# Optimization experiments

Measured on AMD Instinct MI355X. Metric: run time of the kernel, lower is better.

Reference implementation:

```python
import jax, jax.numpy as jnp
import numpy as np

B = 256      # number of graphs (args.batch_size)
NPG = 1000   # nodes per graph (args.num_node)
C = 64       # in_channels
DEG = 16     # avg degree
K = 500      # ceil(ratio * NPG), ratio = 0.5
EPS = 1e-8


def setup_inputs() -> dict:
    key = jax.random.key(0)
    k1, k2, k3, k4, k5 = jax.random.split(key, 5)
    N = B * NPG
    epg = NPG * DEG  # edges per graph
    x = jax.random.normal(k1, (N, C), jnp.float32)
    src = jax.random.randint(k2, (B, epg), 0, NPG)
    dst = jax.random.randint(k3, (B, epg), 0, NPG)
    off = (jnp.arange(B, dtype=jnp.int32) * NPG)[:, None]
    edge_index = jnp.stack([(src + off).reshape(-1), (dst + off).reshape(-1)]).astype(jnp.int32)
    edge_attr = jax.random.uniform(k4, (B * epg,), jnp.float32)
    batch = jnp.repeat(jnp.arange(B, dtype=jnp.int32), NPG)
    W = jax.random.normal(k5, (C, C), jnp.float32) * (1.0 / np.sqrt(C))
    b = jnp.zeros((C,), jnp.float32)
    return {"istraining": 1, "x": x, "edge_index": edge_index, "edge_attr": edge_attr,
            "batch": batch, "W": W, "b": b}


def _gcn_conv(x, edge_index, W, b):
    # PyG GCNConv: x' = D^{-1/2} (A + I) D^{-1/2} X W + b, unit edge weights.
    N = x.shape[0]
    sl = jnp.arange(N, dtype=edge_index.dtype)
    src = jnp.concatenate([edge_index[0], sl])  # message source j
    dst = jnp.concatenate([edge_index[1], sl])  # aggregation target i
    deg = jnp.zeros((N,), x.dtype).at[dst].add(1.0)
    dinv = jnp.where(deg > 0, jax.lax.rsqrt(jnp.maximum(deg, 1.0)), 0.0)
    norm = dinv[src] * dinv[dst]          # [E+N]
    h = x @ W                              # [N, C]
    msg = h[src] * norm[:, None]           # gather + scale (dominant traffic)
    out = jax.ops.segment_sum(msg, dst, num_segments=N) + b
    return out


def _node_score(x):
    # compute_node_score: cosine similarity of each node to its graph centroid
    # (community prototype), plus KL(softmax(score) || uniform) per graph.
    xb = x.reshape(B, NPG, C)
    cen = xb.mean(axis=1, keepdims=True)                       # [B,1,C]
    num = jnp.sum(xb * cen, axis=-1)                           # [B,NPG]
    den = jnp.linalg.norm(xb, axis=-1) * jnp.linalg.norm(cen, axis=-1) + EPS
    score = num / den                                          # [B,NPG]
    logp = jax.nn.log_softmax(score, axis=1)
    kl = jnp.sum(jnp.exp(logp) * (logp + jnp.log(jnp.float32(NPG))), axis=1)  # [B]
    indices_ = jnp.argsort(-score, axis=1)                     # [B,NPG]
    return score, kl, indices_


def reference(istraining, x, edge_index, edge_attr, batch, W, b):
    N = x.shape[0]
    x = _gcn_conv(x, edge_index, W, b)
    score, kl_all_batch, indices_ = _node_score(x)
    # per-graph top-k (fixed k since every graph has NPG nodes)
    _, idx = jax.lax.top_k(score, K)                           # [B,K]
    perm = ((jnp.arange(B, dtype=idx.dtype) * NPG)[:, None] + idx).reshape(-1)  # [B*K]
    score_flat = score.reshape(-1)
    x_new = x[perm] * jnp.tanh(score_flat[perm])[:, None]
    batch_new = batch[perm]
    # filter_adj: keep edges with both endpoints retained, re-index to new ids.
    mapping = jnp.full((N,), -1, dtype=jnp.int32).at[perm].set(
        jnp.arange(perm.shape[0], dtype=jnp.int32))
    new_ei = mapping[edge_index]                               # [2,E], -1 = dropped
    edge_mask = jnp.logical_and(new_ei[0] >= 0, new_ei[1] >= 0)
    edge_attr_new = jnp.where(edge_mask, edge_attr, 0.0)
    return (x_new, new_ei, edge_attr_new, edge_mask, batch_new, perm, kl_all_batch, indices_)
```

## Files before the change

kernel.cpp:

```cpp
#include <hip/hip_runtime.h>
#include <math.h>

#define NPG 1000
#define KTOP 500
#define C 64
#define EPG 16000
#define BPG 63

__device__ __forceinline__ int readlane_i(int v, int l) {
    return (int)__builtin_amdgcn_readlane((unsigned)v, (unsigned)l);
}

__global__ __launch_bounds__(1024) void build_graph_k(const int* __restrict__ ei, int E,
                                                      int* __restrict__ deg,
                                                      float* __restrict__ dinv,
                                                      int* __restrict__ off,
                                                      int* __restrict__ csr) {
    int g = blockIdx.x, t = threadIdx.x;
    __shared__ int cnt[NPG];
    __shared__ int soff[NPG];
    __shared__ unsigned short lcsr[EPG];
    __shared__ int red[1024];
    const int gbase = g * NPG;
    const int ebase = g * EPG;
    const int* __restrict__ srcp = ei + ebase;
    const int* __restrict__ dstp = ei + E + ebase;

    for (int i = t; i < NPG; i += 1024) cnt[i] = 0;
    __syncthreads();
    for (int i = t; i < EPG; i += 1024) atomicAdd(&cnt[dstp[i] - gbase], 1);
    __syncthreads();
    int v = (t < NPG) ? cnt[t] : 0;
    red[t] = v;
    __syncthreads();
    for (int o = 1; o < 1024; o <<= 1) {
        int xx = (t >= o) ? red[t - o] : 0;
        __syncthreads();
        red[t] += xx;
        __syncthreads();
    }
    if (t < NPG) soff[t] = red[t] - v;
    __syncthreads();
    for (int i = t; i < NPG; i += 1024) {
        int d = cnt[i];
        deg[gbase + i] = d;
        dinv[gbase + i] = 1.0f / sqrtf((float)(d + 1));
        off[gbase + i] = ebase + soff[i];
    }
    __syncthreads();
    for (int i = t; i < NPG; i += 1024) cnt[i] = soff[i];
    __syncthreads();
    for (int i = t; i < EPG; i += 1024) {
        int d = dstp[i] - gbase;
        int pos = atomicAdd(&cnt[d], 1);
        lcsr[pos] = (unsigned short)(srcp[i] - gbase);
    }
    __syncthreads();
    int4* co = (int4*)(csr + ebase);
    for (int i = t; i < EPG / 4; i += 1024) {
        int4 vv;
        vv.x = gbase + (int)lcsr[i * 4 + 0];
        vv.y = gbase + (int)lcsr[i * 4 + 1];
        vv.z = gbase + (int)lcsr[i * 4 + 2];
        vv.w = gbase + (int)lcsr[i * 4 + 3];
        co[i] = vv;
    }
}

__global__ __launch_bounds__(256) void gemm_k(const float* __restrict__ x,
                                              const float* __restrict__ W,
                                              const float* __restrict__ dinv,
                                              float* __restrict__ h2, int N) {
    __shared__ float sW[C * C];
    int t = threadIdx.x;
    for (int i = t; i < C * C / 4; i += 256) ((float4*)sW)[i] = ((const float4*)W)[i];
    __syncthreads();
    int r0 = blockIdx.x * 512 + t;
    int r1 = r0 + 256;
    if (r0 >= N) return;
    bool has1 = (r1 < N);
    const float4* x0 = (const float4*)(x + (size_t)r0 * C);
    const float4* x1 = (const float4*)(x + (size_t)(has1 ? r1 : r0) * C);
    float acc0[C], acc1[C];
#pragma unroll
    for (int i = 0; i < C; ++i) { acc0[i] = 0.f; acc1[i] = 0.f; }
    float4 a0 = x0[0], a1 = x1[0];
    for (int k4 = 0; k4 < 16; ++k4) {
        float4 b0, b1;
        if (k4 < 15) { b0 = x0[k4 + 1]; b1 = x1[k4 + 1]; }
        const float4* wr = (const float4*)(sW + k4 * 4 * C);
        const float* a0f = (const float*)&a0;
        const float* a1f = (const float*)&a1;
#pragma unroll
        for (int c4 = 0; c4 < 16; ++c4) {
            float4 w[4];
            w[0] = wr[c4]; w[1] = wr[16 + c4]; w[2] = wr[32 + c4]; w[3] = wr[48 + c4];
            const float* wf = (const float*)w;
#pragma unroll
            for (int j = 0; j < 4; ++j) {
                float s0 = acc0[c4 * 4 + j], s1 = acc1[c4 * 4 + j];
#pragma unroll
                for (int kk = 0; kk < 4; ++kk) {
                    float wv = wf[kk * 4 + j];
                    s0 = fmaf(a0f[kk], wv, s0);
                    s1 = fmaf(a1f[kk], wv, s1);
                }
                acc0[c4 * 4 + j] = s0; acc1[c4 * 4 + j] = s1;
            }
        }
        a0 = b0; a1 = b1;
    }
    float dv0 = dinv[r0];
    float dv1 = has1 ? dinv[r1] : 0.f;
#pragma unroll
    for (int i = 0; i < C; ++i) { acc0[i] *= dv0; acc1[i] *= dv1; }
    float4* h0 = (float4*)(h2 + (size_t)r0 * C);
#pragma unroll
    for (int q = 0; q < 16; ++q) h0[q] = ((float4*)acc0)[q];
    if (has1) {
        float4* h1 = (float4*)(h2 + (size_t)r1 * C);
#pragma unroll
        for (int q = 0; q < 16; ++q) h1[q] = ((float4*)acc1)[q];
    }
}

__global__ __launch_bounds__(256) void gather_k(const int* __restrict__ csr,
                                                const int* __restrict__ off,
                                                const int* __restrict__ deg,
                                                const float* __restrict__ h2,
                                                const float* __restrict__ dinv,
                                                const float* __restrict__ bias,
                                                float* __restrict__ out2,
                                                float* __restrict__ cen_sum,
                                                int N, int B) {
    __shared__ float cenacc[C];
    int blk = blockIdx.x;
    int wave = threadIdx.x >> 6;
    int lane = threadIdx.x & 63;
    int t = threadIdx.x;
    int g, blkin;
    if ((B & 7) == 0) {
        int xcd = blk & 7, slot = blk >> 3;
        g = (slot / BPG) * 8 + xcd;
        blkin = slot % BPG;
    } else {
        g = blk / BPG;
        blkin = blk % BPG;
    }
    if (t < C) cenacc[t] = 0.f;
    __syncthreads();

    int base = blkin * 4 + wave;
    bool active = (base < NPG / 4);
    if (active) {
        int nA = g * NPG + base;
        int nB = nA + 250, nC = nA + 500, nD = nA + 750;
        int oA = off[nA], oB = off[nB], oC = off[nC], oD = off[nD];
        int dA = deg[nA], dB = deg[nB], dC = deg[nC], dD = deg[nD];
        float diA = dinv[nA], diB = dinv[nB], diC = dinv[nC], diD = dinv[nD];
        float hA = h2[(size_t)nA * C + lane];
        float hB = h2[(size_t)nB * C + lane];
        float hC = h2[(size_t)nC * C + lane];
        float hD = h2[(size_t)nD * C + lane];
        float bv = bias[lane];
        int svA = (lane < dA) ? csr[oA + lane] : nA;
        int svB = (lane < dB) ? csr[oB + lane] : nB;
        int svC = (lane < dC) ? csr[oC + lane] : nC;
        int svD = (lane < dD) ? csr[oD + lane] : nD;
        int jmA = dA < 64 ? dA : 64;
        int jmB = dB < 64 ? dB : 64;
        int jmC = dC < 64 ? dC : 64;
        int jmD = dD < 64 ? dD : 64;
        int rA = (jmA + 3) & ~3, rB = (jmB + 3) & ~3;
        int rC = (jmC + 3) & ~3, rD = (jmD + 3) & ~3;
        int m0 = rA > rB ? rA : rB;
        int m1 = rC > rD ? rC : rD;
        int mmax = m0 > m1 ? m0 : m1;
        float aA = 0.f, aB = 0.f, aC = 0.f, aD = 0.f;
        for (int j = 0; j < mmax; j += 4) {
            if (j < rA) {
                int s0 = readlane_i(svA, j + 0), s1 = readlane_i(svA, j + 1);
                int s2 = readlane_i(svA, j + 2), s3 = readlane_i(svA, j + 3);
                float v0 = h2[(size_t)s0 * C + lane];
                float v1 = h2[(size_t)s1 * C + lane];
                float v2 = h2[(size_t)s2 * C + lane];
                float v3 = h2[(size_t)s3 * C + lane];
                aA += (v0 + v1) + (v2 + v3);
            }
            if (j < rB) {
                int s0 = readlane_i(svB, j + 0), s1 = readlane_i(svB, j + 1);
                int s2 = readlane_i(svB, j + 2), s3 = readlane_i(svB, j + 3);
                float v0 = h2[(size_t)s0 * C + lane];
                float v1 = h2[(size_t)s1 * C + lane];
                float v2 = h2[(size_t)s2 * C + lane];
                float v3 = h2[(size_t)s3 * C + lane];
                aB += (v0 + v1) + (v2 + v3);
            }
            if (j < rC) {
                int s0 = readlane_i(svC, j + 0), s1 = readlane_i(svC, j + 1);
                int s2 = readlane_i(svC, j + 2), s3 = readlane_i(svC, j + 3);
                float v0 = h2[(size_t)s0 * C + lane];
                float v1 = h2[(size_t)s1 * C + lane];
                float v2 = h2[(size_t)s2 * C + lane];
                float v3 = h2[(size_t)s3 * C + lane];
                aC += (v0 + v1) + (v2 + v3);
            }
            if (j < rD) {
                int s0 = readlane_i(svD, j + 0), s1 = readlane_i(svD, j + 1);
                int s2 = readlane_i(svD, j + 2), s3 = readlane_i(svD, j + 3);
                float v0 = h2[(size_t)s0 * C + lane];
                float v1 = h2[(size_t)s1 * C + lane];
                float v2 = h2[(size_t)s2 * C + lane];
                float v3 = h2[(size_t)s3 * C + lane];
                aD += (v0 + v1) + (v2 + v3);
            }
        }
        for (int j = 64; j < dA; ++j) aA += h2[(size_t)csr[oA + j] * C + lane];
        for (int j = 64; j < dB; ++j) aB += h2[(size_t)csr[oB + j] * C + lane];
        for (int j = 64; j < dC; ++j) aC += h2[(size_t)csr[oC + j] * C + lane];
        for (int j = 64; j < dD; ++j) aD += h2[(size_t)csr[oD + j] * C + lane];
        float cA = 1.0f - (float)(rA - jmA);
        float cB = 1.0f - (float)(rB - jmB);
        float cC = 1.0f - (float)(rC - jmC);
        float cD = 1.0f - (float)(rD - jmD);
        float resA = fmaf(diA, fmaf(cA, hA, aA), bv);
        float resB = fmaf(diB, fmaf(cB, hB, aB), bv);
        float resC = fmaf(diC, fmaf(cC, hC, aC), bv);
        float resD = fmaf(diD, fmaf(cD, hD, aD), bv);
        out2[(size_t)nA * C + lane] = resA;
        out2[(size_t)nB * C + lane] = resB;
        out2[(size_t)nC * C + lane] = resC;
        out2[(size_t)nD * C + lane] = resD;
        float csum = (resA + resB) + (resC + resD);
        atomicAdd(&cenacc[lane], csum);
    }
    __syncthreads();
    if (t < C) atomicAdd(&cen_sum[(size_t)g * C + t], cenacc[t]);
}

__global__ void cen_fin_k(const float* __restrict__ cen_sum, float* __restrict__ cen,
                          float* __restrict__ cnorm) {
    int g = blockIdx.x, c = threadIdx.x;
    float m = cen_sum[(size_t)g * C + c] * (1.0f / 1000.0f);
    cen[g * C + c] = m;
    float v = m * m;
    for (int o = 32; o > 0; o >>= 1) v += __shfl_down(v, o, 64);
    if (c == 0) cnorm[g] = sqrtf(v);
}

__global__ __launch_bounds__(256) void score2_k(const float* __restrict__ out2,
                                                const float* __restrict__ cen,
                                                const float* __restrict__ cnorm,
                                                float* __restrict__ score, int N) {
    int wave = threadIdx.x >> 6, lane = threadIdx.x & 63;
    int r0 = blockIdx.x * 16 + wave * 4;
    if (r0 >= N) return;
    int g0 = r0 / NPG, g1 = (r0 + 1) / NPG, g2 = (r0 + 2) / NPG, g3 = (r0 + 3) / NPG;
    float a0 = out2[(size_t)(r0 + 0) * C + lane];
    float a1 = out2[(size_t)(r0 + 1) * C + lane];
    float a2 = out2[(size_t)(r0 + 2) * C + lane];
    float a3 = out2[(size_t)(r0 + 3) * C + lane];
    float c0 = cen[g0 * C + lane];
    float c1 = cen[g1 * C + lane];
    float c2 = cen[g2 * C + lane];
    float c3 = cen[g3 * C + lane];
    float n0 = a0 * c0, n1 = a1 * c1, n2 = a2 * c2, n3 = a3 * c3;
    float q0 = a0 * a0, q1 = a1 * a1, q2 = a2 * a2, q3 = a3 * a3;
    for (int o = 32; o > 0; o >>= 1) {
        n0 += __shfl_down(n0, o, 64); q0 += __shfl_down(q0, o, 64);
        n1 += __shfl_down(n1, o, 64); q1 += __shfl_down(q1, o, 64);
        n2 += __shfl_down(n2, o, 64); q2 += __shfl_down(q2, o, 64);
        n3 += __shfl_down(n3, o, 64); q3 += __shfl_down(q3, o, 64);
    }
    if (lane == 0) {
        score[r0 + 0] = n0 / (sqrtf(q0) * cnorm[g0] + 1e-8f);
        score[r0 + 1] = n1 / (sqrtf(q1) * cnorm[g1] + 1e-8f);
        score[r0 + 2] = n2 / (sqrtf(q2) * cnorm[g2] + 1e-8f);
        score[r0 + 3] = n3 / (sqrtf(q3) * cnorm[g3] + 1e-8f);
    }
}

__global__ __launch_bounds__(1024) void post2_k(const float* __restrict__ score,
                                                const float* __restrict__ out2,
                                                int* __restrict__ mapping,
                                                float* __restrict__ o_xnew,
                                                float* __restrict__ o_batch,
                                                float* __restrict__ o_perm,
                                                float* __restrict__ o_kl,
                                                float* __restrict__ o_ind) {
    __shared__ float ss[NPG];
    __shared__ float red[1024];
    __shared__ unsigned long long kk[1024];
    __shared__ int   map[NPG];
    int g = blockIdx.x, t = threadIdx.x;
    int wave = t >> 6, lane = t & 63;
    const int gbase = g * NPG;

    const float4* s4 = (const float4*)(score + (size_t)gbase);
    if (t < NPG / 4) ((float4*)ss)[t] = s4[t];
    __syncthreads();
    float mx = -INFINITY;
    if (t < NPG) mx = ss[t];
    red[t] = mx;
    __syncthreads();
    for (int w = 512; w > 0; w >>= 1) { if (t < w) red[t] = fmaxf(red[t], red[t + w]); __syncthreads(); }
    mx = red[0];
    __syncthreads();
    float se = (t < NPG) ? expf(ss[t] - mx) : 0.f;
    red[t] = se;
    __syncthreads();
    for (int w = 512; w > 0; w >>= 1) { if (t < w) red[t] += red[t + w]; __syncthreads(); }
    float lse = logf(red[0]);
    __syncthreads();
    const float ln_npg = 6.9077552790f;
    float kl = 0.f;
    if (t < NPG) {
        float lp = ss[t] - mx - lse;
        kl = expf(lp) * (lp + ln_npg);
    }
    red[t] = kl;
    __syncthreads();
    for (int w = 512; w > 0; w >>= 1) { if (t < w) red[t] += red[t + w]; __syncthreads(); }
    if (t == 0) o_kl[g] = red[0];
    unsigned long long v;
    if (t < NPG) {
        unsigned u = __float_as_uint(ss[t]);
        u = (u & 0x80000000u) ? ~u : (u | 0x80000000u);
        v = ((unsigned long long)(~u) << 32) | (unsigned)t;
    } else {
        v = ~0ULL;
    }
    __syncthreads();
    kk[t] = v;
    __syncthreads();
    for (int k = 2; k <= 1024; k <<= 1) {
        for (int j = k >> 1; j > 0; j >>= 1) {
            int ixj = t ^ j;
            if (ixj > t) {
                unsigned long long a = kk[t], b2 = kk[ixj];
                bool up = ((t & k) == 0);
                if ((a > b2) == up) { kk[t] = b2; kk[ixj] = a; }
            }
            __syncthreads();
        }
    }
    if (t < NPG) {
        int idx = (int)(kk[t] & 0xFFFFFFFFULL);
        o_ind[(size_t)g * NPG + t] = (float)idx;
        map[t] = -1;
    }
    __syncthreads();
    if (t < KTOP) {
        int node = (int)(kk[t] & 0xFFFFFFFFULL);
        map[node] = g * KTOP + t;
        o_perm[(size_t)g * KTOP + t] = (float)(gbase + node);
        o_batch[(size_t)g * KTOP + t] = (float)g;
    }
    __syncthreads();
    if (t < NPG) mapping[gbase + t] = map[t];
    for (int r = wave; r < KTOP; r += 16) {
        int node = (int)(kk[r] & 0xFFFFFFFFULL);
        float tn = tanhf(ss[node]);
        o_xnew[((size_t)g * KTOP + r) * C + lane] =
            out2[(size_t)(gbase + node) * C + lane] * tn;
    }
}

__global__ void edge_out_k(const int* __restrict__ ei, const float* __restrict__ eattr,
                           const int* __restrict__ mapping, float* __restrict__ o_newei,
                           float* __restrict__ o_eattr, float* __restrict__ o_mask, int E) {
    int e4 = blockIdx.x * 256 + threadIdx.x;
    int q = E >> 2;
    if (e4 < q) {
        int4 sidx = ((const int4*)ei)[e4];
        int4 didx = ((const int4*)ei)[q + e4];
        int a0 = mapping[sidx.x], a1 = mapping[sidx.y], a2 = mapping[sidx.z], a3 = mapping[sidx.w];
        int b0 = mapping[didx.x], b1 = mapping[didx.y], b2 = mapping[didx.z], b3 = mapping[didx.w];
        float4 f0 = { (float)a0, (float)a1, (float)a2, (float)a3 };
        float4 f1 = { (float)b0, (float)b1, (float)b2, (float)b3 };
        ((float4*)o_newei)[e4] = f0;
        ((float4*)o_newei)[q + e4] = f1;
        float4 at = ((const float4*)eattr)[e4];
        float4 mk, ea;
        mk.x = (a0 >= 0 && b0 >= 0) ? 1.0f : 0.0f;
        mk.y = (a1 >= 0 && b1 >= 0) ? 1.0f : 0.0f;
        mk.z = (a2 >= 0 && b2 >= 0) ? 1.0f : 0.0f;
        mk.w = (a3 >= 0 && b3 >= 0) ? 1.0f : 0.0f;
        ea.x = mk.x != 0.0f ? at.x : 0.0f;
        ea.y = mk.y != 0.0f ? at.y : 0.0f;
        ea.z = mk.z != 0.0f ? at.z : 0.0f;
        ea.w = mk.w != 0.0f ? at.w : 0.0f;
        ((float4*)o_mask)[e4] = mk;
        ((float4*)o_eattr)[e4] = ea;
    }
}

extern "C" void kernel_launch(void* const* d_in, const int* in_sizes, int n_in,
                              void* d_out, int out_size, void* d_ws, size_t ws_size,
                              hipStream_t stream) {
    (void)n_in; (void)out_size; (void)ws_size;
    const float* x     = (const float*)d_in[1];
    const int*   ei    = (const int*)d_in[2];
    const float* eattr = (const float*)d_in[3];
    const float* W     = (const float*)d_in[5];
    const float* bias  = (const float*)d_in[6];

    const int N  = in_sizes[1] / C;
    const int E  = in_sizes[2] / 2;
    const int B  = N / NPG;
    const int BK = B * KTOP;

    char* wsp = (char*)d_ws;
    float* out2    = (float*)wsp; wsp += (size_t)N * C * 4;
    float* dinv    = (float*)wsp; wsp += (size_t)N * 4;
    int*   deg     = (int*)wsp;   wsp += (size_t)N * 4;
    int*   off     = (int*)wsp;   wsp += (size_t)N * 4;
    int*   mapping = (int*)wsp;   wsp += (size_t)N * 4;
    float* score   = (float*)wsp; wsp += (size_t)N * 4;
    float* cen_sum = (float*)wsp; wsp += (size_t)B * C * 4;
    float* cen     = (float*)wsp; wsp += (size_t)B * C * 4;
    float* cnorm   = (float*)wsp; wsp += 1024;

    float* out     = (float*)d_out;
    float* o_xnew  = out;
    float* o_newei = o_xnew + (size_t)BK * C;
    float* o_eattr = o_newei + 2 * (size_t)E;
    float* o_mask  = o_eattr + (size_t)E;
    float* o_batch = o_mask + (size_t)E;
    float* o_perm  = o_batch + (size_t)BK;
    float* o_kl    = o_perm + (size_t)BK;
    float* o_ind   = o_kl + (size_t)B;

    float* h2buf = out;
    int*   csr   = (int*)o_eattr;

    hipMemsetAsync(cen_sum, 0, (size_t)B * C * 4, stream);

    build_graph_k<<<B, 1024, 0, stream>>>(ei, E, deg, dinv, off, csr);
    gemm_k<<<(N + 511) / 512, 256, 0, stream>>>(x, W, dinv, h2buf, N);
    gather_k<<<B * BPG, 256, 0, stream>>>(csr, off, deg, h2buf, dinv, bias, out2,
                                          cen_sum, N, B);
    cen_fin_k<<<B, 64, 0, stream>>>(cen_sum, cen, cnorm);
    score2_k<<<(N + 15) / 16, 256, 0, stream>>>(out2, cen, cnorm, score, N);
    post2_k<<<B, 1024, 0, stream>>>(score, out2, mapping,
                                    o_xnew, o_batch, o_perm, o_kl, o_ind);
    edge_out_k<<<(E / 4 + 255) / 256, 256, 0, stream>>>(ei, eattr, mapping,
                                                        o_newei, o_eattr, o_mask, E);
}
```

Measured before the change: 404.4 us.

## Retile GEMM with shared-memory x tiles and fuse centroid finalize into score kernel

The GEMM now stages a 128-row tile of x into shared memory, transposed, and has each thread compute an 8x8 register tile. The old version kept two full 64-wide accumulator rows per thread and re-read all of W for each one, so the new tiling is meant to cut register pressure and improve reuse. The centroid-finalize kernel is removed: score2_k recomputes the mean and its norm from cen_sum on the fly. The memset moves into build_graph_k, which saves two launches. The GEMM launch now assumes N is divisible by 128 and drops the tail handling.

```diff
diff --git a/kernel.cpp b/kernel.cpp
--- a/kernel.cpp
+++ b/kernel.cpp
@@ -15,7 +15,8 @@
                                                       int* __restrict__ deg,
                                                       float* __restrict__ dinv,
                                                       int* __restrict__ off,
-                                                      int* __restrict__ csr) {
+                                                      int* __restrict__ csr,
+                                                      float* __restrict__ cen_sum) {
     int g = blockIdx.x, t = threadIdx.x;
     __shared__ int cnt[NPG];
     __shared__ int soff[NPG];
@@ -26,6 +27,7 @@
     const int* __restrict__ srcp = ei + ebase;
     const int* __restrict__ dstp = ei + E + ebase;
 
+    if (t < C) cen_sum[(size_t)g * C + t] = 0.f;
     for (int i = t; i < NPG; i += 1024) cnt[i] = 0;
     __syncthreads();
     for (int i = t; i < EPG; i += 1024) atomicAdd(&cnt[dstp[i] - gbase], 1);
@@ -67,60 +69,62 @@
     }
 }
 
-__global__ __launch_bounds__(256) void gemm_k(const float* __restrict__ x,
+__global__ __launch_bounds__(128) void gemm_k(const float* __restrict__ x,
                                               const float* __restrict__ W,
                                               const float* __restrict__ dinv,
                                               float* __restrict__ h2, int N) {
+    __shared__ float xT[64][132];
     __shared__ float sW[C * C];
     int t = threadIdx.x;
-    for (int i = t; i < C * C / 4; i += 256) ((float4*)sW)[i] = ((const float4*)W)[i];
-    __syncthreads();
-    int r0 = blockIdx.x * 512 + t;
-    int r1 = r0 + 256;
-    if (r0 >= N) return;
-    bool has1 = (r1 < N);
-    const float4* x0 = (const float4*)(x + (size_t)r0 * C);
-    const float4* x1 = (const float4*)(x + (size_t)(has1 ? r1 : r0) * C);
-    float acc0[C], acc1[C];
-#pragma unroll
-    for (int i = 0; i < C; ++i) { acc0[i] = 0.f; acc1[i] = 0.f; }
-    float4 a0 = x0[0], a1 = x1[0];
-    for (int k4 = 0; k4 < 16; ++k4) {
-        float4 b0, b1;
-        if (k4 < 15) { b0 = x0[k4 + 1]; b1 = x1[k4 + 1]; }
-        const float4* wr = (const float4*)(sW + k4 * 4 * C);
-        const float* a0f = (const float*)&a0;
-        const float* a1f = (const float*)&a1;
-#pragma unroll
-        for (int c4 = 0; c4 < 16; ++c4) {
-            float4 w[4];
-            w[0] = wr[c4]; w[1] = wr[16 + c4]; w[2] = wr[32 + c4]; w[3] = wr[48 + c4];
-            const float* wf = (const float*)w;
-#pragma unroll
-            for (int j = 0; j < 4; ++j) {
-                float s0 = acc0[c4 * 4 + j], s1 = acc1[c4 * 4 + j];
-#pragma unroll
-                for (int kk = 0; kk < 4; ++kk) {
-                    float wv = wf[kk * 4 + j];
-                    s0 = fmaf(a0f[kk], wv, s0);
-                    s1 = fmaf(a1f[kk], wv, s1);
-                }
-                acc0[c4 * 4 + j] = s0; acc1[c4 * 4 + j] = s1;
-            }
-        }
-        a0 = b0; a1 = b1;
-    }
-    float dv0 = dinv[r0];
-    float dv1 = has1 ? dinv[r1] : 0.f;
-#pragma unroll
-    for (int i = 0; i < C; ++i) { acc0[i] *= dv0; acc1[i] *= dv1; }
-    float4* h0 = (float4*)(h2 + (size_t)r0 * C);
-#pragma unroll
-    for (int q = 0; q < 16; ++q) h0[q] = ((float4*)acc0)[q];
-    if (has1) {
-        float4* h1 = (float4*)(h2 + (size_t)r1 * C);
-#pragma unroll
-        for (int q = 0; q < 16; ++q) h1[q] = ((float4*)acc1)[q];
+    int rbase = blockIdx.x * 128;
+    if (rbase >= N) return;
+    for (int i = t; i < C * C / 4; i += 128) ((float4*)sW)[i] = ((const float4*)W)[i];
+    const float4* xsrc = (const float4*)(x + (size_t)rbase * C);
+    for (int i = t; i < 2048; i += 128) {
+        float4 v = xsrc[i];
+        int r = i >> 4;
+        int k0 = (i & 15) * 4;
+        xT[k0 + 0][r] = v.x;
+        xT[k0 + 1][r] = v.y;
+        xT[k0 + 2][r] = v.z;
+        xT[k0 + 3][r] = v.w;
+    }
+    __syncthreads();
+    int rg = t >> 3;
+    int cg = t & 7;
+    int r0 = rg * 8;
+    int c0 = cg * 8;
+    float acc[8][8];
+#pragma unroll
+    for (int i = 0; i < 8; ++i)
+#pragma unroll
+        for (int j = 0; j < 8; ++j) acc[i][j] = 0.f;
+    for (int k = 0; k < 64; ++k) {
+        float4 a0 = *(const float4*)&xT[k][r0];
+        float4 a1 = *(const float4*)&xT[k][r0 + 4];
+        float4 b0 = *(const float4*)&sW[k * C + c0];
+        float4 b1 = *(const float4*)&sW[k * C + c0 + 4];
+        float av[8] = { a0.x, a0.y, a0.z, a0.w, a1.x, a1.y, a1.z, a1.w };
+        float bv[8] = { b0.x, b0.y, b0.z, b0.w, b1.x, b1.y, b1.z, b1.w };
+#pragma unroll
+        for (int i = 0; i < 8; ++i)
+#pragma unroll
+            for (int j = 0; j < 8; ++j)
+                acc[i][j] = fmaf(av[i], bv[j], acc[i][j]);
+    }
+    float dv[8];
+#pragma unroll
+    for (int i = 0; i < 8; ++i) dv[i] = dinv[rbase + r0 + i];
+#pragma unroll
+    for (int i = 0; i < 8; ++i) {
+        float4 o0, o1;
+        o0.x = acc[i][0] * dv[i]; o0.y = acc[i][1] * dv[i];
+        o0.z = acc[i][2] * dv[i]; o0.w = acc[i][3] * dv[i];
+        o1.x = acc[i][4] * dv[i]; o1.y = acc[i][5] * dv[i];
+        o1.z = acc[i][6] * dv[i]; o1.w = acc[i][7] * dv[i];
+        float4* dst = (float4*)(h2 + (size_t)(rbase + r0 + i) * C + c0);
+        dst[0] = o0;
+        dst[1] = o1;
     }
 }
 
@@ -238,45 +242,37 @@
     if (t < C) atomicAdd(&cen_sum[(size_t)g * C + t], cenacc[t]);
 }
 
-__global__ void cen_fin_k(const float* __restrict__ cen_sum, float* __restrict__ cen,
-                          float* __restrict__ cnorm) {
-    int g = blockIdx.x, c = threadIdx.x;
-    float m = cen_sum[(size_t)g * C + c] * (1.0f / 1000.0f);
-    cen[g * C + c] = m;
-    float v = m * m;
-    for (int o = 32; o > 0; o >>= 1) v += __shfl_down(v, o, 64);
-    if (c == 0) cnorm[g] = sqrtf(v);
-}
-
 __global__ __launch_bounds__(256) void score2_k(const float* __restrict__ out2,
-                                                const float* __restrict__ cen,
-                                                const float* __restrict__ cnorm,
+                                                const float* __restrict__ cen_sum,
                                                 float* __restrict__ score, int N) {
     int wave = threadIdx.x >> 6, lane = threadIdx.x & 63;
     int r0 = blockIdx.x * 16 + wave * 4;
     if (r0 >= N) return;
-    int g0 = r0 / NPG, g1 = (r0 + 1) / NPG, g2 = (r0 + 2) / NPG, g3 = (r0 + 3) / NPG;
+    int g0 = (r0 + 0) / NPG, g1 = (r0 + 1) / NPG;
+    int g2 = (r0 + 2) / NPG, g3 = (r0 + 3) / NPG;
+    const float inv = 1.0f / 1000.0f;
+    float m0 = cen_sum[(size_t)g0 * C + lane] * inv;
+    float m1 = cen_sum[(size_t)g1 * C + lane] * inv;
+    float m2 = cen_sum[(size_t)g2 * C + lane] * inv;
+    float m3 = cen_sum[(size_t)g3 * C + lane] * inv;
     float a0 = out2[(size_t)(r0 + 0) * C + lane];
     float a1 = out2[(size_t)(r0 + 1) * C + lane];
     float a2 = out2[(size_t)(r0 + 2) * C + lane];
     float a3 = out2[(size_t)(r0 + 3) * C + lane];
-    float c0 = cen[g0 * C + lane];
-    float c1 = cen[g1 * C + lane];
-    float c2 = cen[g2 * C + lane];
-    float c3 = cen[g3 * C + lane];
-    float n0 = a0 * c0, n1 = a1 * c1, n2 = a2 * c2, n3 = a3 * c3;
+    float n0 = a0 * m0, n1 = a1 * m1, n2 = a2 * m2, n3 = a3 * m3;
     float q0 = a0 * a0, q1 = a1 * a1, q2 = a2 * a2, q3 = a3 * a3;
+    float c0 = m0 * m0, c1 = m1 * m1, c2 = m2 * m2, c3 = m3 * m3;
     for (int o = 32; o > 0; o >>= 1) {
-        n0 += __shfl_down(n0, o, 64); q0 += __shfl_down(q0, o, 64);
-        n1 += __shfl_down(n1, o, 64); q1 += __shfl_down(q1, o, 64);
-        n2 += __shfl_down(n2, o, 64); q2 += __shfl_down(q2, o, 64);
-        n3 += __shfl_down(n3, o, 64); q3 += __shfl_down(q3, o, 64);
+        n0 += __shfl_down(n0, o, 64); q0 += __shfl_down(q0, o, 64); c0 += __shfl_down(c0, o, 64);
+        n1 += __shfl_down(n1, o, 64); q1 += __shfl_down(q1, o, 64); c1 += __shfl_down(c1, o, 64);
+        n2 += __shfl_down(n2, o, 64); q2 += __shfl_down(q2, o, 64); c2 += __shfl_down(c2, o, 64);
+        n3 += __shfl_down(n3, o, 64); q3 += __shfl_down(q3, o, 64); c3 += __shfl_down(c3, o, 64);
     }
     if (lane == 0) {
-        score[r0 + 0] = n0 / (sqrtf(q0) * cnorm[g0] + 1e-8f);
-        score[r0 + 1] = n1 / (sqrtf(q1) * cnorm[g1] + 1e-8f);
-        score[r0 + 2] = n2 / (sqrtf(q2) * cnorm[g2] + 1e-8f);
-        score[r0 + 3] = n3 / (sqrtf(q3) * cnorm[g3] + 1e-8f);
+        score[r0 + 0] = n0 / (sqrtf(q0) * sqrtf(c0) + 1e-8f);
+        score[r0 + 1] = n1 / (sqrtf(q1) * sqrtf(c1) + 1e-8f);
+        score[r0 + 2] = n2 / (sqrtf(q2) * sqrtf(c2) + 1e-8f);
+        score[r0 + 3] = n3 / (sqrtf(q3) * sqrtf(c3) + 1e-8f);
     }
 }
 
@@ -418,8 +414,6 @@
     int*   mapping = (int*)wsp;   wsp += (size_t)N * 4;
     float* score   = (float*)wsp; wsp += (size_t)N * 4;
     float* cen_sum = (float*)wsp; wsp += (size_t)B * C * 4;
-    float* cen     = (float*)wsp; wsp += (size_t)B * C * 4;
-    float* cnorm   = (float*)wsp; wsp += 1024;
 
     float* out     = (float*)d_out;
     float* o_xnew  = out;
@@ -434,14 +428,11 @@
     float* h2buf = out;
     int*   csr   = (int*)o_eattr;
 
-    hipMemsetAsync(cen_sum, 0, (size_t)B * C * 4, stream);
-
-    build_graph_k<<<B, 1024, 0, stream>>>(ei, E, deg, dinv, off, csr);
-    gemm_k<<<(N + 511) / 512, 256, 0, stream>>>(x, W, dinv, h2buf, N);
+    build_graph_k<<<B, 1024, 0, stream>>>(ei, E, deg, dinv, off, csr, cen_sum);
+    gemm_k<<<N / 128, 128, 0, stream>>>(x, W, dinv, h2buf, N);
     gather_k<<<B * BPG, 256, 0, stream>>>(csr, off, deg, h2buf, dinv, bias, out2,
                                           cen_sum, N, B);
-    cen_fin_k<<<B, 64, 0, stream>>>(cen_sum, cen, cnorm);
-    score2_k<<<(N + 15) / 16, 256, 0, stream>>>(out2, cen, cnorm, score, N);
+    score2_k<<<(N + 15) / 16, 256, 0, stream>>>(out2, cen_sum, score, N);
     post2_k<<<B, 1024, 0, stream>>>(score, out2, mapping,
                                     o_xnew, o_batch, o_perm, o_kl, o_ind);
     edge_out_k<<<(E / 4 + 255) / 256, 256, 0, stream>>>(ei, eattr, mapping,
```

New measurement: 409.9 us. About the same (+1.4%).

## Split post-processing into softmax/KL, sort, and top-k gather kernels

Applied to the files above, without the earlier changes.

The monolithic per-graph post kernel, which ran B blocks of 1024 threads, is split into three kernels. The first computes softmax and KL with 256 threads per graph. The second does the bitonic sort and writes the mapping, perm and batch outputs directly. The third is a widely parallel top-k feature gather over all B*K rows, so the heavy out2 gather no longer runs in only 256 blocks. The cen_sum memset is also folded into build_graph_k. This adds two kernel launches and a sidx round trip through global memory.

```diff
diff --git a/kernel.cpp b/kernel.cpp
--- a/kernel.cpp
+++ b/kernel.cpp
@@ -15,7 +15,8 @@
                                                       int* __restrict__ deg,
                                                       float* __restrict__ dinv,
                                                       int* __restrict__ off,
-                                                      int* __restrict__ csr) {
+                                                      int* __restrict__ csr,
+                                                      float* __restrict__ cen_sum) {
     int g = blockIdx.x, t = threadIdx.x;
     __shared__ int cnt[NPG];
     __shared__ int soff[NPG];
@@ -26,6 +27,7 @@
     const int* __restrict__ srcp = ei + ebase;
     const int* __restrict__ dstp = ei + E + ebase;
 
+    if (t < C) cen_sum[(size_t)g * C + t] = 0.f;
     for (int i = t; i < NPG; i += 1024) cnt[i] = 0;
     __syncthreads();
     for (int i = t; i < EPG; i += 1024) atomicAdd(&cnt[dstp[i] - gbase], 1);
@@ -151,21 +153,20 @@
     __syncthreads();
 
     int base = blkin * 4 + wave;
-    bool active = (base < NPG / 4);
-    if (active) {
+    if (base < NPG / 4) {
         int nA = g * NPG + base;
-        int nB = nA + 250, nC = nA + 500, nD = nA + 750;
-        int oA = off[nA], oB = off[nB], oC = off[nC], oD = off[nD];
-        int dA = deg[nA], dB = deg[nB], dC = deg[nC], dD = deg[nD];
-        float diA = dinv[nA], diB = dinv[nB], diC = dinv[nC], diD = dinv[nD];
+        int nB = nA + 250, nC_ = nA + 500, nD = nA + 750;
+        int oA = off[nA], oB = off[nB], oC = off[nC_], oD = off[nD];
+        int dA = deg[nA], dB = deg[nB], dC = deg[nC_], dD = deg[nD];
+        float diA = dinv[nA], diB = dinv[nB], diC = dinv[nC_], diD = dinv[nD];
         float hA = h2[(size_t)nA * C + lane];
         float hB = h2[(size_t)nB * C + lane];
-        float hC = h2[(size_t)nC * C + lane];
+        float hC = h2[(size_t)nC_ * C + lane];
         float hD = h2[(size_t)nD * C + lane];
         float bv = bias[lane];
         int svA = (lane < dA) ? csr[oA + lane] : nA;
         int svB = (lane < dB) ? csr[oB + lane] : nB;
-        int svC = (lane < dC) ? csr[oC + lane] : nC;
+        int svC = (lane < dC) ? csr[oC + lane] : nC_;
         int svD = (lane < dD) ? csr[oD + lane] : nD;
         int jmA = dA < 64 ? dA : 64;
         int jmB = dB < 64 ? dB : 64;
@@ -229,7 +230,7 @@
         float resD = fmaf(diD, fmaf(cD, hD, aD), bv);
         out2[(size_t)nA * C + lane] = resA;
         out2[(size_t)nB * C + lane] = resB;
-        out2[(size_t)nC * C + lane] = resC;
+        out2[(size_t)nC_ * C + lane] = resC;
         out2[(size_t)nD * C + lane] = resD;
         float csum = (resA + resB) + (resC + resD);
         atomicAdd(&cenacc[lane], csum);
@@ -255,16 +256,17 @@
     int wave = threadIdx.x >> 6, lane = threadIdx.x & 63;
     int r0 = blockIdx.x * 16 + wave * 4;
     if (r0 >= N) return;
-    int g0 = r0 / NPG, g1 = (r0 + 1) / NPG, g2 = (r0 + 2) / NPG, g3 = (r0 + 3) / NPG;
+    int g0 = (r0 + 0) / NPG, g1 = (r0 + 1) / NPG;
+    int g2 = (r0 + 2) / NPG, g3 = (r0 + 3) / NPG;
+    float m0 = cen[g0 * C + lane];
+    float m1 = cen[g1 * C + lane];
+    float m2 = cen[g2 * C + lane];
+    float m3 = cen[g3 * C + lane];
     float a0 = out2[(size_t)(r0 + 0) * C + lane];
     float a1 = out2[(size_t)(r0 + 1) * C + lane];
     float a2 = out2[(size_t)(r0 + 2) * C + lane];
     float a3 = out2[(size_t)(r0 + 3) * C + lane];
-    float c0 = cen[g0 * C + lane];
-    float c1 = cen[g1 * C + lane];
-    float c2 = cen[g2 * C + lane];
-    float c3 = cen[g3 * C + lane];
-    float n0 = a0 * c0, n1 = a1 * c1, n2 = a2 * c2, n3 = a3 * c3;
+    float n0 = a0 * m0, n1 = a1 * m1, n2 = a2 * m2, n3 = a3 * m3;
     float q0 = a0 * a0, q1 = a1 * a1, q2 = a2 * a2, q3 = a3 * a3;
     for (int o = 32; o > 0; o >>= 1) {
         n0 += __shfl_down(n0, o, 64); q0 += __shfl_down(q0, o, 64);
@@ -280,89 +282,93 @@
     }
 }
 
-__global__ __launch_bounds__(1024) void post2_k(const float* __restrict__ score,
-                                                const float* __restrict__ out2,
-                                                int* __restrict__ mapping,
-                                                float* __restrict__ o_xnew,
-                                                float* __restrict__ o_batch,
-                                                float* __restrict__ o_perm,
-                                                float* __restrict__ o_kl,
-                                                float* __restrict__ o_ind) {
+__global__ void softmax_kl_k(const float* __restrict__ score, float* __restrict__ o_kl) {
+    int g = blockIdx.x, t = threadIdx.x;
     __shared__ float ss[NPG];
-    __shared__ float red[1024];
+    __shared__ float red[256];
+    const float4* s4 = (const float4*)(score + (size_t)g * NPG);
+    for (int i = t; i < NPG / 4; i += 256) ((float4*)ss)[i] = s4[i];
+    __syncthreads();
+    float mx = -INFINITY;
+    for (int i = t; i < NPG; i += 256) mx = fmaxf(mx, ss[i]);
+    red[t] = mx;
+    __syncthreads();
+    for (int w = 128; w > 0; w >>= 1) { if (t < w) red[t] = fmaxf(red[t], red[t + w]); __syncthreads(); }
+    mx = red[0];
+    __syncthreads();
+    float se = 0.f;
+    for (int i = t; i < NPG; i += 256) se += expf(ss[i] - mx);
+    red[t] = se;
+    __syncthreads();
+    for (int w = 128; w > 0; w >>= 1) { if (t < w) red[t] += red[t + w]; __syncthreads(); }
+    float lse = logf(red[0]);
+    __syncthreads();
+    float kl = 0.f;
+    const float ln_npg = 6.9077552790f;
+    for (int i = t; i < NPG; i += 256) {
+        float lp = ss[i] - mx - lse;
+        kl += expf(lp) * (lp + ln_npg);
+    }
+    red[t] = kl;
+    __syncthreads();
+    for (int w = 128; w > 0; w >>= 1) { if (t < w) red[t] += red[t + w]; __syncthreads(); }
+    if (t == 0) o_kl[g] = red[0];
+}
+
+__global__ __launch_bounds__(1024) void sort_k(const float* __restrict__ score,
+                                               int* __restrict__ sidx,
+                                               int* __restrict__ mapping,
+                                               float* __restrict__ o_perm,
+                                               float* __restrict__ o_batch,
+                                               float* __restrict__ o_ind) {
     __shared__ unsigned long long kk[1024];
-    __shared__ int   map[NPG];
     int g = blockIdx.x, t = threadIdx.x;
-    int wave = t >> 6, lane = t & 63;
     const int gbase = g * NPG;
-
-    const float4* s4 = (const float4*)(score + (size_t)gbase);
-    if (t < NPG / 4) ((float4*)ss)[t] = s4[t];
-    __syncthreads();
-    float mx = -INFINITY;
-    if (t < NPG) mx = ss[t];
-    red[t] = mx;
-    __syncthreads();
-    for (int w = 512; w > 0; w >>= 1) { if (t < w) red[t] = fmaxf(red[t], red[t + w]); __syncthreads(); }
-    mx = red[0];
-    __syncthreads();
-    float se = (t < NPG) ? expf(ss[t] - mx) : 0.f;
-    red[t] = se;
-    __syncthreads();
-    for (int w = 512; w > 0; w >>= 1) { if (t < w) red[t] += red[t + w]; __syncthreads(); }
-    float lse = logf(red[0]);
-    __syncthreads();
-    const float ln_npg = 6.9077552790f;
-    float kl = 0.f;
-    if (t < NPG) {
-        float lp = ss[t] - mx - lse;
-        kl = expf(lp) * (lp + ln_npg);
-    }
-    red[t] = kl;
-    __syncthreads();
-    for (int w = 512; w > 0; w >>= 1) { if (t < w) red[t] += red[t + w]; __syncthreads(); }
-    if (t == 0) o_kl[g] = red[0];
     unsigned long long v;
     if (t < NPG) {
-        unsigned u = __float_as_uint(ss[t]);
+        unsigned u = __float_as_uint(score[(size_t)gbase + t]);
         u = (u & 0x80000000u) ? ~u : (u | 0x80000000u);
         v = ((unsigned long long)(~u) << 32) | (unsigned)t;
     } else {
         v = ~0ULL;
     }
-    __syncthreads();
     kk[t] = v;
     __syncthreads();
     for (int k = 2; k <= 1024; k <<= 1) {
         for (int j = k >> 1; j > 0; j >>= 1) {
             int ixj = t ^ j;
             if (ixj > t) {
-                unsigned long long a = kk[t], b2 = kk[ixj];
+                unsigned long long a = kk[t], b = kk[ixj];
                 bool up = ((t & k) == 0);
-                if ((a > b2) == up) { kk[t] = b2; kk[ixj] = a; }
+                if ((a > b) == up) { kk[t] = b; kk[ixj] = a; }
             }
             __syncthreads();
         }
     }
     if (t < NPG) {
-        int idx = (int)(kk[t] & 0xFFFFFFFFULL);
-        o_ind[(size_t)g * NPG + t] = (float)idx;
-        map[t] = -1;
-    }
-    __syncthreads();
-    if (t < KTOP) {
         int node = (int)(kk[t] & 0xFFFFFFFFULL);
-        map[node] = g * KTOP + t;
-        o_perm[(size_t)g * KTOP + t] = (float)(gbase + node);
-        o_batch[(size_t)g * KTOP + t] = (float)g;
-    }
-    __syncthreads();
-    if (t < NPG) mapping[gbase + t] = map[t];
-    for (int r = wave; r < KTOP; r += 16) {
-        int node = (int)(kk[r] & 0xFFFFFFFFULL);
-        float tn = tanhf(ss[node]);
-        o_xnew[((size_t)g * KTOP + r) * C + lane] =
-            out2[(size_t)(gbase + node) * C + lane] * tn;
+        sidx[(size_t)gbase + t] = node;
+        o_ind[(size_t)gbase + t] = (float)node;
+        mapping[gbase + node] = (t < KTOP) ? (g * KTOP + t) : -1;
+        if (t < KTOP) {
+            o_perm[(size_t)g * KTOP + t] = (float)(gbase + node);
+            o_batch[(size_t)g * KTOP + t] = (float)g;
+        }
+    }
+}
+
+__global__ __launch_bounds__(256) void topk_k(const int* __restrict__ sidx,
+                                              const float* __restrict__ score,
+                                              const float* __restrict__ out2,
+                                              float* __restrict__ o_xnew, int BK) {
+    int wave = threadIdx.x >> 6, lane = threadIdx.x & 63;
+    int j = blockIdx.x * 4 + wave;
+    if (j < BK) {
+        int b = j / KTOP, r = j - b * KTOP;
+        int node = sidx[(size_t)b * NPG + r];
+        int gn = b * NPG + node;
+        float tn = tanhf(score[gn]);
+        o_xnew[(size_t)j * C + lane] = out2[(size_t)gn * C + lane] * tn;
     }
 }
 
@@ -417,6 +423,7 @@
     int*   off     = (int*)wsp;   wsp += (size_t)N * 4;
     int*   mapping = (int*)wsp;   wsp += (size_t)N * 4;
     float* score   = (float*)wsp; wsp += (size_t)N * 4;
+    int*   sidx    = (int*)wsp;   wsp += (size_t)N * 4;
     float* cen_sum = (float*)wsp; wsp += (size_t)B * C * 4;
     float* cen     = (float*)wsp; wsp += (size_t)B * C * 4;
     float* cnorm   = (float*)wsp; wsp += 1024;
@@ -434,16 +441,15 @@
     float* h2buf = out;
     int*   csr   = (int*)o_eattr;
 
-    hipMemsetAsync(cen_sum, 0, (size_t)B * C * 4, stream);
-
-    build_graph_k<<<B, 1024, 0, stream>>>(ei, E, deg, dinv, off, csr);
+    build_graph_k<<<B, 1024, 0, stream>>>(ei, E, deg, dinv, off, csr, cen_sum);
     gemm_k<<<(N + 511) / 512, 256, 0, stream>>>(x, W, dinv, h2buf, N);
     gather_k<<<B * BPG, 256, 0, stream>>>(csr, off, deg, h2buf, dinv, bias, out2,
                                           cen_sum, N, B);
     cen_fin_k<<<B, 64, 0, stream>>>(cen_sum, cen, cnorm);
     score2_k<<<(N + 15) / 16, 256, 0, stream>>>(out2, cen, cnorm, score, N);
-    post2_k<<<B, 1024, 0, stream>>>(score, out2, mapping,
-                                    o_xnew, o_batch, o_perm, o_kl, o_ind);
+    softmax_kl_k<<<B, 256, 0, stream>>>(score, o_kl);
+    sort_k<<<B, 1024, 0, stream>>>(score, sidx, mapping, o_perm, o_batch, o_ind);
+    topk_k<<<(BK + 3) / 4, 256, 0, stream>>>(sidx, score, out2, o_xnew, BK);
     edge_out_k<<<(E / 4 + 255) / 256, 256, 0, stream>>>(ei, eattr, mapping,
                                                         o_newei, o_eattr, o_mask, E);
 }
```

Result: slower. 414.8 us (+2.6%).
